# Performance work log

Hardware: AMD Instinct MI355X
Metric: run time of the kernel (lower is better)

## Reference

```python
import jax, jax.numpy as jnp
import numpy as np

FLOAT_MIN = np.float32(np.finfo(np.float32).min)  # torch.finfo().min for float32
K_DIM = 64  # init kwarg, equals head dim of query/key


def setup_inputs() -> dict:
    key = jax.random.key(0)
    k1, k2, k3, k4 = jax.random.split(key, 4)
    B, Lq, Lk, D, Dv = 16, 2048, 2048, 64, 64
    return {
        "query": jax.random.normal(k1, (B, Lq, D), dtype=jnp.float32),
        "key": jax.random.normal(k2, (B, Lk, D), dtype=jnp.float32),
        "value": jax.random.normal(k3, (B, Lk, Dv), dtype=jnp.float32),
        "mask": jax.random.uniform(k4, (1, Lq, Lk), dtype=jnp.float32),
    }


def reference(query, key, value, mask):
    # scores: [B, Lq, Lk]
    scores = jnp.einsum("bqd,bkd->bqk", query, key) / jnp.sqrt(jnp.float32(K_DIM))
    # multiplicative mask -> additive log-bias, clamped at float32 min
    scores = scores + jnp.maximum(jnp.log(mask), FLOAT_MIN)
    # NOTE: source applies softmax over dim=1 (the query axis), faithfully reproduced
    attn = jax.nn.softmax(scores, axis=1)
    return jnp.einsum("bqk,bkv->bqv", attn, value)
```

## Files before the change

kernel.cpp:

```cpp
#include <hip/hip_runtime.h>
#include <cstdint>
#include <cstddef>


#define LSEQ 2048
#define DHEAD 64

typedef __bf16 v8bf __attribute__((ext_vector_type(8)));
typedef __bf16 v4bf __attribute__((ext_vector_type(4)));
typedef float v4f __attribute__((ext_vector_type(4)));

#define MFMA16(a, b, c) __builtin_amdgcn_mfma_f32_16x16x32_bf16(a, b, c, 0, 0, 0)

#if __has_builtin(__builtin_amdgcn_exp2f)
#define EXP2F(x) __builtin_amdgcn_exp2f(x)
#else
#define EXP2F(x) __expf((x) * 0.6931471805599453f)
#endif

__device__ __forceinline__ void gl_lds16(const void* g, void* l) {
  __builtin_amdgcn_global_load_lds(
      (__attribute__((address_space(1))) void*)g,
      (__attribute__((address_space(3))) void*)l, 16, 0, 0);
}

__global__ __launch_bounds__(256) void cast_qk(const float* __restrict__ Q,
                                               const float* __restrict__ K,
                                               __bf16* __restrict__ Qb,
                                               __bf16* __restrict__ Kb) {
  const float S = 0.18033688011112042f;
  size_t i = ((size_t)blockIdx.x * 256 + threadIdx.x) * 4;
  float4 q = *(const float4*)(Q + i);
  float4 k = *(const float4*)(K + i);
  v4bf qo = {(__bf16)(q.x * S), (__bf16)(q.y * S), (__bf16)(q.z * S), (__bf16)(q.w * S)};
  v4bf ko = {(__bf16)k.x, (__bf16)k.y, (__bf16)k.z, (__bf16)k.w};
  *(v4bf*)(Qb + i) = qo;
  *(v4bf*)(Kb + i) = ko;
}

__global__ __launch_bounds__(256) void stats_k(const __bf16* __restrict__ Qb,
                                               const __bf16* __restrict__ Kb,
                                               const float* __restrict__ mask,
                                               float* __restrict__ Lpart) {
  const int bx = blockIdx.x;
  const int b = bx >> 7;
  const int qc = (bx >> 5) & 3;
  const int k0 = (bx & 31) * 64;
  const int tid = threadIdx.x;
  const int wave = tid >> 6, lane = tid & 63;
  const int quad = lane >> 4, n = lane & 15;

  __shared__ __align__(16) __bf16 Qt[64 * 64];
  __shared__ __align__(16) float psum[4][64];

  v8bf ak[4][2];
#pragma unroll
  for (int sub = 0; sub < 4; ++sub)
#pragma unroll
    for (int dh = 0; dh < 2; ++dh)
      ak[sub][dh] = *(const v8bf*)(Kb + ((size_t)b * LSEQ + k0 + sub * 16 + n) * DHEAD +
                                   dh * 32 + quad * 8);

  float colsum[4][4];
#pragma unroll
  for (int s = 0; s < 4; ++s)
#pragma unroll
    for (int r = 0; r < 4; ++r) colsum[s][r] = 0.f;

  const int qbeg = qc * 512;
  for (int q0 = qbeg; q0 < qbeg + 512; q0 += 64) {
    __syncthreads();
#pragma unroll
    for (int i = 0; i < 2; ++i) {
      int s = (wave * 2 + i) * 64 + lane;
      int row = s >> 3, gc = (s & 7) ^ (row & 7);
      gl_lds16(Qb + ((size_t)b * LSEQ + q0 + row) * DHEAD + gc * 8, &Qt[s * 8]);
    }
    __syncthreads();

    v8bf bq[2];
    const int qr = wave * 16 + n;
#pragma unroll
    for (int dh = 0; dh < 2; ++dh)
      bq[dh] = *(const v8bf*)&Qt[qr * 64 + ((dh * 4 + quad) ^ (qr & 7)) * 8];

#pragma unroll
    for (int sub = 0; sub < 4; ++sub) {
      v4f c = {0.f, 0.f, 0.f, 0.f};
      c = MFMA16(ak[sub][0], bq[0], c);
      c = MFMA16(ak[sub][1], bq[1], c);
      const float4 m4 = *(const float4*)&mask[(size_t)(q0 + wave * 16 + n) * LSEQ +
                                              k0 + sub * 16 + quad * 4];
#pragma unroll
      for (int r = 0; r < 4; ++r)
        colsum[sub][r] += ((const float*)&m4)[r] * EXP2F(c[r]);
    }
  }

#pragma unroll
  for (int sub = 0; sub < 4; ++sub) {
#pragma unroll
    for (int r = 0; r < 4; ++r) {
      float v = colsum[sub][r];
      v += __shfl_xor(v, 1);
      v += __shfl_xor(v, 2);
      v += __shfl_xor(v, 4);
      v += __shfl_xor(v, 8);
      colsum[sub][r] = v;
    }
    if (n == 0) {
      v4f w = {colsum[sub][0], colsum[sub][1], colsum[sub][2], colsum[sub][3]};
      *(v4f*)&psum[wave][sub * 16 + quad * 4] = w;
    }
  }
  __syncthreads();
  if (tid < 64) {
    float s = psum[0][tid] + psum[1][tid] + psum[2][tid] + psum[3][tid];
    Lpart[((size_t)b * LSEQ + k0 + tid) * 4 + qc] = s;
  }
}

__global__ __launch_bounds__(256) void vtrans_k(const float* __restrict__ V,
                                                const float* __restrict__ Lpart,
                                                __bf16* __restrict__ Vts) {
  const int b = blockIdx.x >> 6;
  const int k0 = (blockIdx.x & 63) * 32;
  const int tid = threadIdx.x;
  __shared__ float tile[32][65];
  __shared__ float invl[32];
  if (tid < 32) {
    float4 lp = *(const float4*)&Lpart[((size_t)b * LSEQ + k0 + tid) * 4];
    invl[tid] = 1.0f / (lp.x + lp.y + lp.z + lp.w);
  }
#pragma unroll
  for (int t = 0; t < 8; ++t) {
    int flat = t * 256 + tid;
    int k = flat >> 6, v = flat & 63;
    tile[k][v] = V[((size_t)b * LSEQ + k0 + k) * DHEAD + v];
  }
  __syncthreads();
#pragma unroll
  for (int t = 0; t < 8; ++t) {
    int flat = t * 256 + tid;
    int v = flat >> 5, k = flat & 31;
    Vts[((size_t)b * DHEAD + v) * LSEQ + k0 + k] = (__bf16)(tile[k][v] * invl[k]);
  }
}

__global__ __launch_bounds__(256) void attn_k(const __bf16* __restrict__ Qb,
                                              const __bf16* __restrict__ Kb,
                                              const __bf16* __restrict__ Vts,
                                              const float* __restrict__ mask,
                                              float* __restrict__ out) {
  const int bx = blockIdx.x;
  const int b = bx >> 7;
  const int kc = (bx >> 5) & 3;
  const int q0 = (bx & 31) * 64;
  const int tid = threadIdx.x;
  const int wave = tid >> 6, lane = tid & 63;
  const int quad = lane >> 4, n = lane & 15;

  __shared__ __align__(16) __bf16 Kt[64 * 64];
  __shared__ __align__(16) __bf16 Vt[64 * 64];
  __shared__ __align__(16) __bf16 Pt[64 * 72];

  v8bf bq[2];
  {
    const int qr = q0 + wave * 16 + n;
#pragma unroll
    for (int dh = 0; dh < 2; ++dh)
      bq[dh] = *(const v8bf*)(Qb + ((size_t)b * LSEQ + qr) * DHEAD + dh * 32 + quad * 8);
  }

  v4f acc[4];
#pragma unroll
  for (int vs = 0; vs < 4; ++vs) acc[vs] = (v4f){0.f, 0.f, 0.f, 0.f};

  const int kbeg = kc * 512;
  for (int k0 = kbeg; k0 < kbeg + 512; k0 += 64) {
    __syncthreads();
#pragma unroll
    for (int i = 0; i < 2; ++i) {
      int s = (wave * 2 + i) * 64 + lane;
      int row = s >> 3, gc = (s & 7) ^ (row & 7);
      gl_lds16(Kb + ((size_t)b * LSEQ + k0 + row) * DHEAD + gc * 8, &Kt[s * 8]);
      gl_lds16(Vts + ((size_t)b * DHEAD + row) * LSEQ + k0 + gc * 8, &Vt[s * 8]);
    }
    __syncthreads();

#pragma unroll
    for (int sub = 0; sub < 4; ++sub) {
      v4f c = {0.f, 0.f, 0.f, 0.f};
      const int kr = sub * 16 + n;
#pragma unroll
      for (int dh = 0; dh < 2; ++dh) {
        v8bf akf = *(const v8bf*)&Kt[kr * 64 + ((dh * 4 + quad) ^ (kr & 7)) * 8];
        c = MFMA16(akf, bq[dh], c);
      }
      const float4 m4 = *(const float4*)&mask[(size_t)(q0 + wave * 16 + n) * LSEQ +
                                              k0 + sub * 16 + quad * 4];
      v4bf pw;
#pragma unroll
      for (int r = 0; r < 4; ++r)
        pw[r] = (__bf16)(((const float*)&m4)[r] * EXP2F(c[r]));
      *(v4bf*)&Pt[(wave * 16 + n) * 72 + sub * 16 + quad * 4] = pw;
    }
    __asm__ volatile("s_waitcnt lgkmcnt(0)" ::: "memory");

#pragma unroll
    for (int kk = 0; kk < 2; ++kk) {
      v8bf ap = *(const v8bf*)&Pt[(wave * 16 + n) * 72 + kk * 32 + quad * 8];
#pragma unroll
      for (int vs = 0; vs < 4; ++vs) {
        const int vr = vs * 16 + n;
        v8bf bv = *(const v8bf*)&Vt[vr * 64 + ((kk * 4 + quad) ^ (vr & 7)) * 8];
        acc[vs] = MFMA16(ap, bv, acc[vs]);
      }
    }
  }

#pragma unroll
  for (int vs = 0; vs < 4; ++vs)
#pragma unroll
    for (int r = 0; r < 4; ++r)
      unsafeAtomicAdd(
          &out[((size_t)b * LSEQ + q0 + wave * 16 + quad * 4 + r) * DHEAD + vs * 16 + n],
          acc[vs][r]);
}

extern "C" void kernel_launch(void* const* d_in, const int* in_sizes, int n_in,
                              void* d_out, int out_size, void* d_ws, size_t ws_size,
                              hipStream_t stream) {
  const float* Q = (const float*)d_in[0];
  const float* K = (const float*)d_in[1];
  const float* V = (const float*)d_in[2];
  const float* mask = (const float*)d_in[3];
  float* out = (float*)d_out;

  char* ws = (char*)d_ws;
  __bf16* Qb = (__bf16*)(ws);
  __bf16* Kb = (__bf16*)(ws + 4194304);
  __bf16* Vts = (__bf16*)(ws + 8388608);
  float* Lpart = (float*)d_out;
  if (ws_size < 12582912) return;

  cast_qk<<<2048, 256, 0, stream>>>(Q, K, Qb, Kb);
  stats_k<<<2048, 256, 0, stream>>>(Qb, Kb, mask, Lpart);
  vtrans_k<<<1024, 256, 0, stream>>>(V, Lpart, Vts);
  hipMemsetAsync(out, 0, (size_t)out_size * sizeof(float), stream);
  attn_k<<<2048, 256, 0, stream>>>(Qb, Kb, Vts, mask, out);
}
```

Before: 212.6 us.

## Drop LDS staging, keep P in registers via 16x16x16 MFMA layout

The stats kernel now loads Q fragments straight from global memory instead of staging them through LDS with barriers. The attention kernel is restructured so each block covers 32 queries and half the keys, with every wave owning its own key slice. The exp(P) tile stays in registers and feeds a 16x16x16 bf16 MFMA directly, removing the LDS round trip for P, K and V and the per-tile syncs. Partial outputs are reduced across waves in LDS before fewer global atomics, at the cost of smaller MFMAs and uncoalesced direct global loads.

New measurement: 319.1 us. 50.1% more time.

```diff
diff --git a/kernel.cpp b/kernel.cpp
--- a/kernel.cpp
+++ b/kernel.cpp
@@ -9,20 +9,24 @@
 typedef __bf16 v8bf __attribute__((ext_vector_type(8)));
 typedef __bf16 v4bf __attribute__((ext_vector_type(4)));
 typedef float v4f __attribute__((ext_vector_type(4)));
-
-#define MFMA16(a, b, c) __builtin_amdgcn_mfma_f32_16x16x32_bf16(a, b, c, 0, 0, 0)
-
-#if __has_builtin(__builtin_amdgcn_exp2f)
+typedef short v4s __attribute__((ext_vector_type(4)));
+
+#define MFMA_QK(a, b, c) __builtin_amdgcn_mfma_f32_16x16x32_bf16(a, b, c, 0, 0, 0)
+
+__device__ __forceinline__ v4f mfma_pv(v4bf a, v4bf b, v4f c) {
+#if defined(__HIP_DEVICE_COMPILE__)
+  return __builtin_amdgcn_mfma_f32_16x16x16bf16_1k(
+      __builtin_bit_cast(v4s, a), __builtin_bit_cast(v4s, b), c, 0, 0, 0);
+#else
+  return c;
+#endif
+}
+
+#if defined(__HIP_DEVICE_COMPILE__)
 #define EXP2F(x) __builtin_amdgcn_exp2f(x)
 #else
-#define EXP2F(x) __expf((x) * 0.6931471805599453f)
+#define EXP2F(x) (x)
 #endif
-
-__device__ __forceinline__ void gl_lds16(const void* g, void* l) {
-  __builtin_amdgcn_global_load_lds(
-      (__attribute__((address_space(1))) void*)g,
-      (__attribute__((address_space(3))) void*)l, 16, 0, 0);
-}
 
 __global__ __launch_bounds__(256) void cast_qk(const float* __restrict__ Q,
                                                const float* __restrict__ K,
@@ -50,7 +54,6 @@
   const int wave = tid >> 6, lane = tid & 63;
   const int quad = lane >> 4, n = lane & 15;
 
-  __shared__ __align__(16) __bf16 Qt[64 * 64];
   __shared__ __align__(16) float psum[4][64];
 
   v8bf ak[4][2];
@@ -61,39 +64,29 @@
       ak[sub][dh] = *(const v8bf*)(Kb + ((size_t)b * LSEQ + k0 + sub * 16 + n) * DHEAD +
                                    dh * 32 + quad * 8);
 
-  float colsum[4][4];
+  float cs[4][4];
 #pragma unroll
   for (int s = 0; s < 4; ++s)
 #pragma unroll
-    for (int r = 0; r < 4; ++r) colsum[s][r] = 0.f;
-
-  const int qbeg = qc * 512;
-  for (int q0 = qbeg; q0 < qbeg + 512; q0 += 64) {
-    __syncthreads();
-#pragma unroll
-    for (int i = 0; i < 2; ++i) {
-      int s = (wave * 2 + i) * 64 + lane;
-      int row = s >> 3, gc = (s & 7) ^ (row & 7);
-      gl_lds16(Qb + ((size_t)b * LSEQ + q0 + row) * DHEAD + gc * 8, &Qt[s * 8]);
-    }
-    __syncthreads();
-
-    v8bf bq[2];
-    const int qr = wave * 16 + n;
-#pragma unroll
-    for (int dh = 0; dh < 2; ++dh)
-      bq[dh] = *(const v8bf*)&Qt[qr * 64 + ((dh * 4 + quad) ^ (qr & 7)) * 8];
-
+    for (int r = 0; r < 4; ++r) cs[s][r] = 0.f;
+
+  const __bf16* qbase = Qb + ((size_t)b * LSEQ + qc * 512 + wave * 16 + n) * DHEAD;
+  const float* mbase = mask + (size_t)(qc * 512 + wave * 16 + n) * LSEQ + k0;
+
+  for (int it = 0; it < 8; ++it) {
+    const __bf16* qp = qbase + (size_t)it * 64 * DHEAD;
+    v8bf bq0 = *(const v8bf*)(qp + quad * 8);
+    v8bf bq1 = *(const v8bf*)(qp + 32 + quad * 8);
+    const float* mp = mbase + (size_t)it * 64 * LSEQ;
 #pragma unroll
     for (int sub = 0; sub < 4; ++sub) {
       v4f c = {0.f, 0.f, 0.f, 0.f};
-      c = MFMA16(ak[sub][0], bq[0], c);
-      c = MFMA16(ak[sub][1], bq[1], c);
-      const float4 m4 = *(const float4*)&mask[(size_t)(q0 + wave * 16 + n) * LSEQ +
-                                              k0 + sub * 16 + quad * 4];
+      c = MFMA_QK(ak[sub][0], bq0, c);
+      c = MFMA_QK(ak[sub][1], bq1, c);
+      const float4 m4 = *(const float4*)(mp + sub * 16 + quad * 4);
 #pragma unroll
       for (int r = 0; r < 4; ++r)
-        colsum[sub][r] += ((const float*)&m4)[r] * EXP2F(c[r]);
+        cs[sub][r] += ((const float*)&m4)[r] * EXP2F(c[r]);
     }
   }
 
@@ -101,15 +94,15 @@
   for (int sub = 0; sub < 4; ++sub) {
 #pragma unroll
     for (int r = 0; r < 4; ++r) {
-      float v = colsum[sub][r];
+      float v = cs[sub][r];
       v += __shfl_xor(v, 1);
       v += __shfl_xor(v, 2);
       v += __shfl_xor(v, 4);
       v += __shfl_xor(v, 8);
-      colsum[sub][r] = v;
+      cs[sub][r] = v;
     }
     if (n == 0) {
-      v4f w = {colsum[sub][0], colsum[sub][1], colsum[sub][2], colsum[sub][3]};
+      v4f w = {cs[sub][0], cs[sub][1], cs[sub][2], cs[sub][3]};
       *(v4f*)&psum[wave][sub * 16 + quad * 4] = w;
     }
   }
@@ -154,78 +147,82 @@
                                               float* __restrict__ out) {
   const int bx = blockIdx.x;
   const int b = bx >> 7;
-  const int kc = (bx >> 5) & 3;
-  const int q0 = (bx & 31) * 64;
+  const int kc = (bx >> 6) & 1;
+  const int q0 = (bx & 63) * 32;
   const int tid = threadIdx.x;
   const int wave = tid >> 6, lane = tid & 63;
   const int quad = lane >> 4, n = lane & 15;
 
-  __shared__ __align__(16) __bf16 Kt[64 * 64];
-  __shared__ __align__(16) __bf16 Vt[64 * 64];
-  __shared__ __align__(16) __bf16 Pt[64 * 72];
-
-  v8bf bq[2];
+  __shared__ __align__(16) float Ored[32][68];
+
+  v8bf bq[2][2];
+#pragma unroll
+  for (int qt = 0; qt < 2; ++qt)
+#pragma unroll
+    for (int dh = 0; dh < 2; ++dh)
+      bq[qt][dh] = *(const v8bf*)(Qb + ((size_t)b * LSEQ + q0 + qt * 16 + n) * DHEAD +
+                                  dh * 32 + quad * 8);
+
+  v4f acc[2][4];
+#pragma unroll
+  for (int qt = 0; qt < 2; ++qt)
+#pragma unroll
+    for (int vt = 0; vt < 4; ++vt) acc[qt][vt] = (v4f){0.f, 0.f, 0.f, 0.f};
+
+  const __bf16* kbase = Kb + ((size_t)b * LSEQ + kc * 1024 + wave * 16 + n) * DHEAD;
+
+  for (int it = 0; it < 16; ++it) {
+    const __bf16* kp = kbase + (size_t)it * 64 * DHEAD;
+    v8bf ak0 = *(const v8bf*)(kp + quad * 8);
+    v8bf ak1 = *(const v8bf*)(kp + 32 + quad * 8);
+
+    const int kb = kc * 1024 + it * 64 + wave * 16 + quad * 4;
+    v4bf av[4];
+#pragma unroll
+    for (int vt = 0; vt < 4; ++vt)
+      av[vt] = *(const v4bf*)(Vts + ((size_t)b * DHEAD + vt * 16 + n) * LSEQ + kb);
+
+#pragma unroll
+    for (int qt = 0; qt < 2; ++qt) {
+      v4f c = {0.f, 0.f, 0.f, 0.f};
+      c = MFMA_QK(ak0, bq[qt][0], c);
+      c = MFMA_QK(ak1, bq[qt][1], c);
+      const float4 m4 = *(const float4*)(mask + (size_t)(q0 + qt * 16 + n) * LSEQ + kb);
+      v4bf pb;
+#pragma unroll
+      for (int r = 0; r < 4; ++r)
+        pb[r] = (__bf16)(((const float*)&m4)[r] * EXP2F(c[r]));
+#pragma unroll
+      for (int vt = 0; vt < 4; ++vt) acc[qt][vt] = mfma_pv(av[vt], pb, acc[qt][vt]);
+    }
+  }
+
+#pragma unroll 1
+  for (int w = 0; w < 4; ++w) {
+    if (wave == w) {
+#pragma unroll
+      for (int qt = 0; qt < 2; ++qt)
+#pragma unroll
+        for (int vt = 0; vt < 4; ++vt) {
+          float* p = &Ored[qt * 16 + n][vt * 16 + quad * 4];
+          if (w == 0)
+            *(v4f*)p = acc[qt][vt];
+          else {
+            v4f t = *(v4f*)p;
+            t += acc[qt][vt];
+            *(v4f*)p = t;
+          }
+        }
+    }
+    __syncthreads();
+  }
+
   {
-    const int qr = q0 + wave * 16 + n;
-#pragma unroll
-    for (int dh = 0; dh < 2; ++dh)
-      bq[dh] = *(const v8bf*)(Qb + ((size_t)b * LSEQ + qr) * DHEAD + dh * 32 + quad * 8);
-  }
-
-  v4f acc[4];
-#pragma unroll
-  for (int vs = 0; vs < 4; ++vs) acc[vs] = (v4f){0.f, 0.f, 0.f, 0.f};
-
-  const int kbeg = kc * 512;
-  for (int k0 = kbeg; k0 < kbeg + 512; k0 += 64) {
-    __syncthreads();
-#pragma unroll
-    for (int i = 0; i < 2; ++i) {
-      int s = (wave * 2 + i) * 64 + lane;
-      int row = s >> 3, gc = (s & 7) ^ (row & 7);
-      gl_lds16(Kb + ((size_t)b * LSEQ + k0 + row) * DHEAD + gc * 8, &Kt[s * 8]);
-      gl_lds16(Vts + ((size_t)b * DHEAD + row) * LSEQ + k0 + gc * 8, &Vt[s * 8]);
-    }
-    __syncthreads();
-
-#pragma unroll
-    for (int sub = 0; sub < 4; ++sub) {
-      v4f c = {0.f, 0.f, 0.f, 0.f};
-      const int kr = sub * 16 + n;
-#pragma unroll
-      for (int dh = 0; dh < 2; ++dh) {
-        v8bf akf = *(const v8bf*)&Kt[kr * 64 + ((dh * 4 + quad) ^ (kr & 7)) * 8];
-        c = MFMA16(akf, bq[dh], c);
-      }
-      const float4 m4 = *(const float4*)&mask[(size_t)(q0 + wave * 16 + n) * LSEQ +
-                                              k0 + sub * 16 + quad * 4];
-      v4bf pw;
-#pragma unroll
-      for (int r = 0; r < 4; ++r)
-        pw[r] = (__bf16)(((const float*)&m4)[r] * EXP2F(c[r]));
-      *(v4bf*)&Pt[(wave * 16 + n) * 72 + sub * 16 + quad * 4] = pw;
-    }
-    __asm__ volatile("s_waitcnt lgkmcnt(0)" ::: "memory");
-
-#pragma unroll
-    for (int kk = 0; kk < 2; ++kk) {
-      v8bf ap = *(const v8bf*)&Pt[(wave * 16 + n) * 72 + kk * 32 + quad * 8];
-#pragma unroll
-      for (int vs = 0; vs < 4; ++vs) {
-        const int vr = vs * 16 + n;
-        v8bf bv = *(const v8bf*)&Vt[vr * 64 + ((kk * 4 + quad) ^ (vr & 7)) * 8];
-        acc[vs] = MFMA16(ap, bv, acc[vs]);
-      }
-    }
-  }
-
-#pragma unroll
-  for (int vs = 0; vs < 4; ++vs)
-#pragma unroll
-    for (int r = 0; r < 4; ++r)
-      unsafeAtomicAdd(
-          &out[((size_t)b * LSEQ + q0 + wave * 16 + quad * 4 + r) * DHEAD + vs * 16 + n],
-          acc[vs][r]);
+    const int q = tid >> 3, vb = (tid & 7) * 8;
+    float* op = &out[((size_t)b * LSEQ + q0 + q) * DHEAD + vb];
+#pragma unroll
+    for (int i = 0; i < 8; ++i) unsafeAtomicAdd(op + i, Ored[q][vb + i]);
+  }
 }
 
 extern "C" void kernel_launch(void* const* d_in, const int* in_sizes, int n_in,
@@ -247,6 +244,6 @@
   cast_qk<<<2048, 256, 0, stream>>>(Q, K, Qb, Kb);
   stats_k<<<2048, 256, 0, stream>>>(Qb, Kb, mask, Lpart);
   vtrans_k<<<1024, 256, 0, stream>>>(V, Lpart, Vts);
-  hipMemsetAsync(out, 0, (size_t)out_size * sizeof(float), stream);
+  (void)hipMemsetAsync(out, 0, (size_t)out_size * sizeof(float), stream);
   attn_k<<<2048, 256, 0, stream>>>(Qb, Kb, Vts, mask, out);
 }
```
